# Kernel optimization log

Measured on AMD Instinct MI355X. Metric: run time of the kernel, lower is better.

The kernel has to match this reference:

```python
import jax, jax.numpy as jnp
import numpy as np

NEG_INF = -1e9
LN_EPS = 1e-5

N, F_IN, F_OUT, H = 4096, 128, 64, 4


def setup_inputs() -> dict:
    key = jax.random.key(0)
    ks = jax.random.split(key, 8)
    return {
        "nodes_features": jax.random.normal(ks[0], (N, F_IN), jnp.float32),
        "degree_matrix": jax.random.normal(ks[1], (N, N), jnp.float32),
        "edges_features_distance": jax.random.normal(ks[2], (N, N), jnp.float32),
        "edges_features_bond": jax.random.normal(ks[3], (N, N), jnp.float32),
        "proj_param": jax.random.normal(ks[4], (H, F_IN, F_OUT), jnp.float32) * 0.1,
        "score_src": jax.random.normal(ks[5], (H, F_OUT, 1), jnp.float32) * 0.1,
        "score_tgt": jax.random.normal(ks[6], (H, F_OUT, 1), jnp.float32) * 0.1,
        "skip_w": jax.random.normal(ks[7], (H * F_OUT, F_IN), jnp.float32) * 0.1,
        "cutoff": 0,
    }


def reference(nodes_features, degree_matrix, edges_features_distance,
              edges_features_bond, proj_param, score_src, score_tgt,
              skip_w, cutoff):
    # connectivity mask: nested where on degree/bond matrices  [N, N]
    wdm = degree_matrix + edges_features_bond
    mask = jnp.where(wdm > 0, wdm,
                     jnp.where(edges_features_bond > cutoff,
                               edges_features_bond + wdm, NEG_INF))

    # per-head projection: [H, N, F_out]
    proj = jnp.einsum('nf,hfo->hno', nodes_features, proj_param)

    # scalar scores per node per head: [H, N, 1]
    s_src = jnp.einsum('hno,hop->hnp', proj, score_src)
    s_tgt = jnp.einsum('hno,hop->hnp', proj, score_tgt)

    # broadcast score matrix [H, N, N]; softmax over dim=1 (as in the original)
    scores = jax.nn.leaky_relu(s_src + jnp.swapaxes(s_tgt, 1, 2), negative_slope=0.2)
    attn = jax.nn.softmax(scores + mask[None, :, :], axis=1)

    # weighted aggregation: [H, N, F_out] -> [N, H, F_out]
    out = jnp.einsum('hij,hjf->hif', attn, proj)
    out = jnp.swapaxes(out, 0, 1)

    # skip connection (F_in != F_out -> linear skip projection)
    skip = (nodes_features @ skip_w.T).reshape(-1, H, F_OUT)
    out = out + skip

    # concat heads, ELU activation (no bias: ctor passes bias=None)
    out = jax.nn.elu(out.reshape(-1, H * F_OUT))

    # fresh LayerNorm (weight=1, bias=0) over last dim of mask
    mu = jnp.mean(mask, axis=-1, keepdims=True)
    var = jnp.var(mask, axis=-1, keepdims=True)
    mask_ln = (mask - mu) / jnp.sqrt(var + LN_EPS)

    return out, mask_ln
```

## Files before the change

### kernel.cpp

```cpp
#include <hip/hip_runtime.h>
#include <math.h>

constexpr int kN  = 4096;
constexpr int kFI = 128;
constexpr int kFO = 64;
constexpr int kH  = 4;
constexpr int kHF = 256;
constexpr float kNegInf = -1e9f;
constexpr float kLnEps  = 1e-5f;

typedef short bf16x8 __attribute__((ext_vector_type(8)));
typedef float f32x4  __attribute__((ext_vector_type(4)));

__device__ __forceinline__ float lrelu(float x){ return x >= 0.f ? x : 0.2f*x; }

__device__ __forceinline__ float wave_sum(float v){
  #pragma unroll
  for (int s = 32; s > 0; s >>= 1) v += __shfl_xor(v, s, 64);
  return v;
}

__device__ __forceinline__ unsigned short f2bf(float x){
  unsigned u = __float_as_uint(x);
  u = (u + 0x7fffu + ((u >> 16) & 1u)) >> 16;
  return (unsigned short)u;
}
__device__ __forceinline__ unsigned f2bf_pk(float a, float b){
  return (unsigned)f2bf(a) | ((unsigned)f2bf(b) << 16);
}

__global__ __launch_bounds__(256) void k_tr(
    const float* __restrict__ skw, float* __restrict__ skwT)
{
  const int k  = blockIdx.x;
  const int hf = threadIdx.x;
  skwT[k*kHF + hf] = skw[hf*kFI + k];
}

__global__ __launch_bounds__(256) void k_proj(
    const float* __restrict__ nodes, const float* __restrict__ pp,
    const float* __restrict__ ssrc,  const float* __restrict__ stgt,
    const float* __restrict__ skwT,
    float* __restrict__ proj, float* __restrict__ ga, float* __restrict__ gb,
    float* __restrict__ skipo)
{
  __shared__ float feat[8][kFI];
  const int tid = threadIdx.x;
  const int n0  = blockIdx.x * 8;
  for (int idx = tid; idx < 8*kFI; idx += 256)
    feat[idx >> 7][idx & 127] = nodes[n0*kFI + idx];
  __syncthreads();
  const int h = tid >> 6, o = tid & 63;
  float accP[8], accS[8];
  #pragma unroll
  for (int n = 0; n < 8; ++n){ accP[n] = 0.f; accS[n] = 0.f; }
  for (int k0 = 0; k0 < kFI; k0 += 4){
    float p[4], w[4];
    #pragma unroll
    for (int u = 0; u < 4; ++u){
      p[u] = pp[(h*kFI + k0+u)*kFO + o];
      w[u] = skwT[(k0+u)*kHF + tid];
    }
    #pragma unroll
    for (int n = 0; n < 8; ++n){
      const float4 f4 = *(const float4*)&feat[n][k0];
      accP[n] = fmaf(f4.x, p[0], fmaf(f4.y, p[1],
                fmaf(f4.z, p[2], fmaf(f4.w, p[3], accP[n]))));
      accS[n] = fmaf(f4.x, w[0], fmaf(f4.y, w[1],
                fmaf(f4.z, w[2], fmaf(f4.w, w[3], accS[n]))));
    }
  }
  const float sa = ssrc[h*kFO + o];
  const float sb = stgt[h*kFO + o];
  #pragma unroll
  for (int n = 0; n < 8; ++n){
    proj[(h*kN + n0+n)*kFO + o] = accP[n];
    skipo[(n0+n)*kHF + tid]     = accS[n];
    const float va = wave_sum(accP[n] * sa);
    const float vb = wave_sum(accP[n] * sb);
    if (o == 0){ ga[h*kN + n0+n] = va; gb[h*kN + n0+n] = vb; }
  }
}

template<int RS>
__global__ __launch_bounds__(256, 6) void k_colsum(
    const float* __restrict__ degm, const float* __restrict__ bondm,
    const float* __restrict__ ga,   const float* __restrict__ gb,
    const int* __restrict__ cutp,
    float* __restrict__ Spart, float* __restrict__ statg,
    float* __restrict__ maskws, int write_mask)
{
  const int j0 = (blockIdx.x * 256 + threadIdx.x) * 4;
  const int lane = threadIdx.x & 63;
  const float cut = (float)cutp[0];
  float4 bv[kH]; f32x4 sv[kH];
  #pragma unroll
  for (int h = 0; h < kH; ++h){
    bv[h] = *(const float4*)&gb[h*kN + j0];
    sv[h] = (f32x4){0.f, 0.f, 0.f, 0.f};
  }
  float msum[RS], msq[RS];
  #pragma unroll
  for (int r = 0; r < RS; ++r){ msum[r] = 0.f; msq[r] = 0.f; }

  const int i0 = blockIdx.y * RS;
  #pragma unroll
  for (int ib = 0; ib < RS; ib += 4){
    float4 dg[4], bd[4];
    #pragma unroll
    for (int u = 0; u < 4; ++u){
      const size_t off = (size_t)(i0+ib+u)*kN + j0;
      dg[u] = *(const float4*)&degm[off];
      bd[u] = *(const float4*)&bondm[off];
    }
    #pragma unroll
    for (int u = 0; u < 4; ++u){
      const int i = i0 + ib + u;
      float4 m;
      {
        float w0 = dg[u].x + bd[u].x, w1 = dg[u].y + bd[u].y;
        float w2 = dg[u].z + bd[u].z, w3 = dg[u].w + bd[u].w;
        m.x = w0 > 0.f ? w0 : (bd[u].x > cut ? bd[u].x + w0 : kNegInf);
        m.y = w1 > 0.f ? w1 : (bd[u].y > cut ? bd[u].y + w1 : kNegInf);
        m.z = w2 > 0.f ? w2 : (bd[u].z > cut ? bd[u].z + w2 : kNegInf);
        m.w = w3 > 0.f ? w3 : (bd[u].w > cut ? bd[u].w + w3 : kNegInf);
      }
      if (write_mask) *(float4*)&maskws[(size_t)i*kN + j0] = m;
      msum[ib+u] += (m.x + m.y) + (m.z + m.w);
      msq[ib+u]  += fmaf(m.x, m.x, fmaf(m.y, m.y, fmaf(m.z, m.z, m.w*m.w)));
      #pragma unroll
      for (int h = 0; h < kH; ++h){
        const float a = ga[h*kN + i];
        sv[h][0] += __expf(lrelu(a + bv[h].x) + m.x);
        sv[h][1] += __expf(lrelu(a + bv[h].y) + m.y);
        sv[h][2] += __expf(lrelu(a + bv[h].z) + m.z);
        sv[h][3] += __expf(lrelu(a + bv[h].w) + m.w);
      }
    }
  }
  #pragma unroll
  for (int h = 0; h < kH; ++h)
    *(float4*)&Spart[(size_t)(blockIdx.y*kH + h)*kN + j0] = *(float4*)&sv[h];

  #pragma unroll
  for (int r = 0; r < RS; ++r){
    const float s1 = wave_sum(msum[r]);
    const float s2 = wave_sum(msq[r]);
    if (lane == 0){
      atomicAdd(&statg[2*(i0+r)+0], s1);
      atomicAdd(&statg[2*(i0+r)+1], s2);
    }
  }
}

__global__ __launch_bounds__(256) void k_sred(
    const float* __restrict__ Spart, float* __restrict__ S, int strips)
{
  __shared__ float red[4][64];
  const int hj0  = blockIdx.x * 64;
  const int lane = threadIdx.x & 63;
  const int g    = threadIdx.x >> 6;
  const int per  = strips >> 2;
  float s0=0.f, s1=0.f, s2=0.f, s3=0.f;
  for (int p = g*per; p < (g+1)*per; p += 4){
    s0 += Spart[(size_t)(p+0)*kH*kN + hj0 + lane];
    s1 += Spart[(size_t)(p+1)*kH*kN + hj0 + lane];
    s2 += Spart[(size_t)(p+2)*kH*kN + hj0 + lane];
    s3 += Spart[(size_t)(p+3)*kH*kN + hj0 + lane];
  }
  red[g][lane] = (s0+s1)+(s2+s3);
  __syncthreads();
  if (threadIdx.x < 64)
    S[hj0+lane] = (red[0][lane]+red[1][lane])+(red[2][lane]+red[3][lane]);
}

__global__ __launch_bounds__(256) void k_stat(
    const float* __restrict__ statg, float* __restrict__ statg2)
{
  const int i = blockIdx.x * 256 + threadIdx.x;
  const float mu  = statg[2*i] * (1.f/kN);
  const float var = statg[2*i+1] * (1.f/kN) - mu*mu;
  statg2[2*i+0] = mu;
  statg2[2*i+1] = rsqrtf(var + kLnEps);
}

__global__ __launch_bounds__(256) void k_pack(
    const float* __restrict__ proj, const float* __restrict__ S,
    unsigned short* __restrict__ pSpack)
{
  const int t = blockIdx.x * 256 + threadIdx.x;
  const int L  = t & 63;
  const int nt = (t >> 6) & 3;
  const int kb = (t >> 8) & 127;
  const int h  = t >> 15;
  const int f  = nt*16 + (L & 15);
  const int jb = kb*32 + (L >> 4)*8;
  union { unsigned short s[8]; uint4 v; } u;
  #pragma unroll
  for (int r = 0; r < 8; ++r){
    const int j = jb + r;
    u.s[r] = f2bf(proj[(size_t)(h*kN + j)*kFO + f] / S[h*kN + j]);
  }
  ((uint4*)pSpack)[t] = u.v;
}

__global__ __launch_bounds__(256) void k_aggr(
    const float* __restrict__ degm, const float* __restrict__ bondm,
    const float* __restrict__ maskws, int have_mask,
    const float* __restrict__ ga, const float* __restrict__ gb,
    const int* __restrict__ cutp,
    const unsigned short* __restrict__ pSpack,
    const float* __restrict__ statg2,
    float* __restrict__ accpart, float* __restrict__ mlnp)
{
  __shared__ unsigned short ebuf[kH*16*70];
  const int tid = threadIdx.x;
  const int w   = tid >> 6;
  const int L   = tid & 63;
  const int r0  = blockIdx.x * 16;
  const int jq  = blockIdx.y;
  const int span = kN / gridDim.y;
  const int nc   = span >> 6;
  const int jq0 = jq * span;
  const int ia  = tid >> 4;
  const int jc  = tid & 15;
  const float cut = (float)cutp[0];

  float av[kH];
  #pragma unroll
  for (int hh = 0; hh < kH; ++hh) av[hh] = ga[hh*kN + r0 + ia];
  const float mu = statg2[2*(r0+ia)+0];
  const float rs = statg2[2*(r0+ia)+1];

  f32x4 acc[4];
  #pragma unroll
  for (int nt = 0; nt < 4; ++nt) acc[nt] = (f32x4){0.f,0.f,0.f,0.f};

  for (int c = 0; c < nc; ++c){
    const int jb = jq0 + c*64;
    {
      const int jg = jb + 4*jc;
      const size_t off = (size_t)(r0+ia)*kN + jg;
      float4 m;
      if (have_mask){
        m = *(const float4*)&maskws[off];
      } else {
        const float4 dg = *(const float4*)&degm[off];
        const float4 bd = *(const float4*)&bondm[off];
        float w0 = dg.x + bd.x, w1 = dg.y + bd.y;
        float w2 = dg.z + bd.z, w3 = dg.w + bd.w;
        m.x = w0 > 0.f ? w0 : (bd.x > cut ? bd.x + w0 : kNegInf);
        m.y = w1 > 0.f ? w1 : (bd.y > cut ? bd.y + w1 : kNegInf);
        m.z = w2 > 0.f ? w2 : (bd.z > cut ? bd.z + w2 : kNegInf);
        m.w = w3 > 0.f ? w3 : (bd.w > cut ? bd.w + w3 : kNegInf);
      }
      float4 o;
      o.x = (m.x - mu) * rs;  o.y = (m.y - mu) * rs;
      o.z = (m.z - mu) * rs;  o.w = (m.w - mu) * rs;
      *(float4*)&mlnp[off] = o;
      #pragma unroll
      for (int hh = 0; hh < kH; ++hh){
        const float4 bv = *(const float4*)&gb[hh*kN + jg];
        const float e0 = __expf(lrelu(av[hh] + bv.x) + m.x);
        const float e1 = __expf(lrelu(av[hh] + bv.y) + m.y);
        const float e2 = __expf(lrelu(av[hh] + bv.z) + m.z);
        const float e3 = __expf(lrelu(av[hh] + bv.w) + m.w);
        uint2 u;
        u.x = f2bf_pk(e0, e1);
        u.y = f2bf_pk(e2, e3);
        *(uint2*)&ebuf[(hh*16 + ia)*70 + 4*jc] = u;
      }
    }
    __syncthreads();
    {
      const int kb0 = (jb >> 5);
      #pragma unroll
      for (int ks = 0; ks < 2; ++ks){
        const bf16x8 a = *(const bf16x8*)&ebuf[(w*16 + (L & 15))*70 + ks*32 + (L >> 4)*8];
        const int kb = kb0 + ks;
        #pragma unroll
        for (int nt = 0; nt < 4; ++nt){
          const bf16x8 b = *(const bf16x8*)&pSpack[(size_t)(((w*128 + kb)*4 + nt)*64 + L)*8];
          acc[nt] = __builtin_amdgcn_mfma_f32_16x16x32_bf16(a, b, acc[nt], 0, 0, 0);
        }
      }
    }
    __syncthreads();
  }

  #pragma unroll
  for (int nt = 0; nt < 4; ++nt){
    #pragma unroll
    for (int reg = 0; reg < 4; ++reg){
      const int i = r0 + (L >> 4)*4 + reg;
      const int f = w*64 + nt*16 + (L & 15);
      accpart[((size_t)jq*kN + i)*kHF + f] = acc[nt][reg];
    }
  }
}

__global__ __launch_bounds__(256) void k_out(
    const float* __restrict__ accpart, const float* __restrict__ skipo,
    float* __restrict__ outp, int nq)
{
  const int idx = blockIdx.x * 256 + threadIdx.x;
  float o = skipo[idx];
  for (int q = 0; q < nq; ++q) o += accpart[(size_t)q*kN*kHF + idx];
  o = o > 0.f ? o : expm1f(o);
  outp[idx] = o;
}

extern "C" void kernel_launch(void* const* d_in, const int* in_sizes, int n_in,
                              void* d_out, int out_size, void* d_ws, size_t ws_size,
                              hipStream_t stream)
{
  const float* nodes = (const float*)d_in[0];
  const float* degm  = (const float*)d_in[1];
  const float* bondm = (const float*)d_in[3];
  const float* pp    = (const float*)d_in[4];
  const float* ssrc  = (const float*)d_in[5];
  const float* stgt  = (const float*)d_in[6];
  const float* skw   = (const float*)d_in[7];
  const int*   cutp  = (const int*)d_in[8];

  const size_t fixed_floats = (size_t)kH*kN*kFO + 3*(size_t)kH*kN
                            + (size_t)kN*kHF + 4*(size_t)kN + (size_t)kFI*kHF;
  const size_t psp_floats = ((size_t)kH*kN*kFO)/2;
  const size_t region8 = (size_t)8*kN*kHF;
  const size_t region4 = (size_t)4*kN*kHF;
  const size_t need8      = (fixed_floats + region8 + psp_floats) * sizeof(float);
  const size_t need8_mask = need8 + (size_t)kN*kN*sizeof(float);
  const size_t need4_mask = (fixed_floats + region4 + psp_floats + (size_t)kN*kN)
                            * sizeof(float);

  int nq, strips, have_mask;
  if (ws_size >= need8_mask)      { nq = 8; strips = 512; have_mask = 1; }
  else if (ws_size >= need8)      { nq = 8; strips = 512; have_mask = 0; }
  else                            { nq = 4; strips = 256;
                                    have_mask = (ws_size >= need4_mask) ? 1 : 0; }

  float* ws     = (float*)d_ws;
  float* proj   = ws;
  float* ga     = proj + (size_t)kH*kN*kFO;
  float* gb     = ga + kH*kN;
  float* S      = gb + kH*kN;
  float* skip   = S + kH*kN;
  float* statg  = skip + (size_t)kN*kHF;
  float* statg2 = statg + 2*kN;
  float* skwT   = statg2 + 2*kN;
  float* accpart= skwT + (size_t)kFI*kHF;
  float* Spart  = accpart;
  unsigned short* pSpack = (unsigned short*)(accpart + (size_t)nq*kN*kHF);
  float* mask   = (float*)(pSpack + (size_t)kH*kN*kFO);

  float* outp = (float*)d_out;
  float* mlnp = outp + (size_t)kN*kHF;

  hipMemsetAsync(statg, 0, 2*kN*sizeof(float), stream);

  k_tr<<<kFI, 256, 0, stream>>>(skw, skwT);
  k_proj<<<kN/8, 256, 0, stream>>>(nodes, pp, ssrc, stgt, skwT, proj, ga, gb, skip);
  if (strips == 512)
    k_colsum<8><<<dim3(kN/1024, 512), 256, 0, stream>>>(degm, bondm, ga, gb, cutp,
                                                        Spart, statg, mask, have_mask);
  else
    k_colsum<16><<<dim3(kN/1024, 256), 256, 0, stream>>>(degm, bondm, ga, gb, cutp,
                                                         Spart, statg, mask, have_mask);
  k_sred<<<(kH*kN)/64, 256, 0, stream>>>(Spart, S, strips);
  k_stat<<<kN/256, 256, 0, stream>>>(statg, statg2);
  k_pack<<<(kH*128*4*64)/256, 256, 0, stream>>>(proj, S, pSpack);
  k_aggr<<<dim3(kN/16, nq), 256, 0, stream>>>(degm, bondm, mask, have_mask,
                                              ga, gb, cutp, pSpack, statg2,
                                              accpart, mlnp);
  k_out<<<(kN*kHF)/256, 256, 0, stream>>>(accpart, skip, outp, nq);
}
```

Baseline: 336.2 us.

## Software-pipeline loads in proj and aggr, use exp2, split S reduction across blocks

k_proj now double-buffers its weight loads and k_aggr prefetches the next chunk's mask and gb values, so global loads overlap with compute. Both exponent sites use exp2f with a folded log2(e) factor and a fmax-based leaky ReLU to cut ALU work. k_colsum drops its occupancy hint and loads 8 rows at a time for more memory-level parallelism. k_sred is split over 8 y-blocks that accumulate into S with atomics, and the workspace is reordered so one memset zeroes both statg and S. The costs are higher register pressure and float atomics that make the summation order nondeterministic.

```diff
diff --git a/kernel.cpp b/kernel.cpp
--- a/kernel.cpp
+++ b/kernel.cpp
@@ -8,6 +8,7 @@
 constexpr int kHF = 256;
 constexpr float kNegInf = -1e9f;
 constexpr float kLnEps  = 1e-5f;
+constexpr float kL2E    = 1.44269504f;
 
 typedef short bf16x8 __attribute__((ext_vector_type(8)));
 typedef float f32x4  __attribute__((ext_vector_type(4)));
@@ -54,22 +55,35 @@
   float accP[8], accS[8];
   #pragma unroll
   for (int n = 0; n < 8; ++n){ accP[n] = 0.f; accS[n] = 0.f; }
-  for (int k0 = 0; k0 < kFI; k0 += 4){
-    float p[4], w[4];
+
+  auto LOADK = [&](int kk, float* p, float* w){
     #pragma unroll
     for (int u = 0; u < 4; ++u){
-      p[u] = pp[(h*kFI + k0+u)*kFO + o];
-      w[u] = skwT[(k0+u)*kHF + tid];
-    }
+      p[u] = pp[(h*kFI + kk+u)*kFO + o];
+      w[u] = skwT[(kk+u)*kHF + tid];
+    }
+  };
+  auto COMP = [&](int kk, const float* p, const float* w){
     #pragma unroll
     for (int n = 0; n < 8; ++n){
-      const float4 f4 = *(const float4*)&feat[n][k0];
+      const float4 f4 = *(const float4*)&feat[n][kk];
       accP[n] = fmaf(f4.x, p[0], fmaf(f4.y, p[1],
                 fmaf(f4.z, p[2], fmaf(f4.w, p[3], accP[n]))));
       accS[n] = fmaf(f4.x, w[0], fmaf(f4.y, w[1],
                 fmaf(f4.z, w[2], fmaf(f4.w, w[3], accS[n]))));
     }
-  }
+  };
+
+  float pA[4], wA[4], pB[4], wB[4];
+  LOADK(0, pA, wA);
+  #pragma unroll
+  for (int k0 = 0; k0 < kFI; k0 += 8){
+    LOADK(k0+4, pB, wB);
+    COMP(k0, pA, wA);
+    if (k0+8 < kFI) LOADK(k0+8, pA, wA);
+    COMP(k0+4, pB, wB);
+  }
+
   const float sa = ssrc[h*kFO + o];
   const float sb = stgt[h*kFO + o];
   #pragma unroll
@@ -83,7 +97,7 @@
 }
 
 template<int RS>
-__global__ __launch_bounds__(256, 6) void k_colsum(
+__global__ __launch_bounds__(256) void k_colsum(
     const float* __restrict__ degm, const float* __restrict__ bondm,
     const float* __restrict__ ga,   const float* __restrict__ gb,
     const int* __restrict__ cutp,
@@ -105,16 +119,16 @@
 
   const int i0 = blockIdx.y * RS;
   #pragma unroll
-  for (int ib = 0; ib < RS; ib += 4){
-    float4 dg[4], bd[4];
-    #pragma unroll
-    for (int u = 0; u < 4; ++u){
+  for (int ib = 0; ib < RS; ib += 8){
+    float4 dg[8], bd[8];
+    #pragma unroll
+    for (int u = 0; u < 8; ++u){
       const size_t off = (size_t)(i0+ib+u)*kN + j0;
       dg[u] = *(const float4*)&degm[off];
       bd[u] = *(const float4*)&bondm[off];
     }
     #pragma unroll
-    for (int u = 0; u < 4; ++u){
+    for (int u = 0; u < 8; ++u){
       const int i = i0 + ib + u;
       float4 m;
       {
@@ -128,13 +142,18 @@
       if (write_mask) *(float4*)&maskws[(size_t)i*kN + j0] = m;
       msum[ib+u] += (m.x + m.y) + (m.z + m.w);
       msq[ib+u]  += fmaf(m.x, m.x, fmaf(m.y, m.y, fmaf(m.z, m.z, m.w*m.w)));
+      const float4 ml = {m.x*kL2E, m.y*kL2E, m.z*kL2E, m.w*kL2E};
       #pragma unroll
       for (int h = 0; h < kH; ++h){
         const float a = ga[h*kN + i];
-        sv[h][0] += __expf(lrelu(a + bv[h].x) + m.x);
-        sv[h][1] += __expf(lrelu(a + bv[h].y) + m.y);
-        sv[h][2] += __expf(lrelu(a + bv[h].z) + m.z);
-        sv[h][3] += __expf(lrelu(a + bv[h].w) + m.w);
+        float t0 = a + bv[h].x, t1 = a + bv[h].y;
+        float t2 = a + bv[h].z, t3 = a + bv[h].w;
+        t0 = fmaxf(t0, 0.2f*t0); t1 = fmaxf(t1, 0.2f*t1);
+        t2 = fmaxf(t2, 0.2f*t2); t3 = fmaxf(t3, 0.2f*t3);
+        sv[h][0] += exp2f(fmaf(t0, kL2E, ml.x));
+        sv[h][1] += exp2f(fmaf(t1, kL2E, ml.y));
+        sv[h][2] += exp2f(fmaf(t2, kL2E, ml.z));
+        sv[h][3] += exp2f(fmaf(t3, kL2E, ml.w));
       }
     }
   }
@@ -160,9 +179,11 @@
   const int hj0  = blockIdx.x * 64;
   const int lane = threadIdx.x & 63;
   const int g    = threadIdx.x >> 6;
-  const int per  = strips >> 2;
+  const int per_chunk = strips >> 3;
+  const int per_wave  = per_chunk >> 2;
+  const int p0 = blockIdx.y*per_chunk + g*per_wave;
   float s0=0.f, s1=0.f, s2=0.f, s3=0.f;
-  for (int p = g*per; p < (g+1)*per; p += 4){
+  for (int p = p0; p < p0 + per_wave; p += 4){
     s0 += Spart[(size_t)(p+0)*kH*kN + hj0 + lane];
     s1 += Spart[(size_t)(p+1)*kH*kN + hj0 + lane];
     s2 += Spart[(size_t)(p+2)*kH*kN + hj0 + lane];
@@ -171,7 +192,8 @@
   red[g][lane] = (s0+s1)+(s2+s3);
   __syncthreads();
   if (threadIdx.x < 64)
-    S[hj0+lane] = (red[0][lane]+red[1][lane])+(red[2][lane]+red[3][lane]);
+    atomicAdd(&S[hj0+lane],
+              (red[0][lane]+red[1][lane])+(red[2][lane]+red[3][lane]));
 }
 
 __global__ __launch_bounds__(256) void k_stat(
@@ -236,43 +258,62 @@
   #pragma unroll
   for (int nt = 0; nt < 4; ++nt) acc[nt] = (f32x4){0.f,0.f,0.f,0.f};
 
+  float4 m_n; float4 bv_n[kH];
+  auto LOADC = [&](int c){
+    const int jg = jq0 + c*64 + 4*jc;
+    const size_t off = (size_t)(r0+ia)*kN + jg;
+    if (have_mask){
+      m_n = *(const float4*)&maskws[off];
+    } else {
+      const float4 dg = *(const float4*)&degm[off];
+      const float4 bd = *(const float4*)&bondm[off];
+      float w0 = dg.x + bd.x, w1 = dg.y + bd.y;
+      float w2 = dg.z + bd.z, w3 = dg.w + bd.w;
+      m_n.x = w0 > 0.f ? w0 : (bd.x > cut ? bd.x + w0 : kNegInf);
+      m_n.y = w1 > 0.f ? w1 : (bd.y > cut ? bd.y + w1 : kNegInf);
+      m_n.z = w2 > 0.f ? w2 : (bd.z > cut ? bd.z + w2 : kNegInf);
+      m_n.w = w3 > 0.f ? w3 : (bd.w > cut ? bd.w + w3 : kNegInf);
+    }
+    #pragma unroll
+    for (int hh = 0; hh < kH; ++hh)
+      bv_n[hh] = *(const float4*)&gb[hh*kN + jg];
+  };
+
+  LOADC(0);
   for (int c = 0; c < nc; ++c){
-    const int jb = jq0 + c*64;
     {
-      const int jg = jb + 4*jc;
+      const float4 m = m_n;
+      float4 bvl[kH];
+      #pragma unroll
+      for (int hh = 0; hh < kH; ++hh) bvl[hh] = bv_n[hh];
+
+      const int jg = jq0 + c*64 + 4*jc;
       const size_t off = (size_t)(r0+ia)*kN + jg;
-      float4 m;
-      if (have_mask){
-        m = *(const float4*)&maskws[off];
-      } else {
-        const float4 dg = *(const float4*)&degm[off];
-        const float4 bd = *(const float4*)&bondm[off];
-        float w0 = dg.x + bd.x, w1 = dg.y + bd.y;
-        float w2 = dg.z + bd.z, w3 = dg.w + bd.w;
-        m.x = w0 > 0.f ? w0 : (bd.x > cut ? bd.x + w0 : kNegInf);
-        m.y = w1 > 0.f ? w1 : (bd.y > cut ? bd.y + w1 : kNegInf);
-        m.z = w2 > 0.f ? w2 : (bd.z > cut ? bd.z + w2 : kNegInf);
-        m.w = w3 > 0.f ? w3 : (bd.w > cut ? bd.w + w3 : kNegInf);
-      }
       float4 o;
       o.x = (m.x - mu) * rs;  o.y = (m.y - mu) * rs;
       o.z = (m.z - mu) * rs;  o.w = (m.w - mu) * rs;
       *(float4*)&mlnp[off] = o;
+      const float4 ml = {m.x*kL2E, m.y*kL2E, m.z*kL2E, m.w*kL2E};
       #pragma unroll
       for (int hh = 0; hh < kH; ++hh){
-        const float4 bv = *(const float4*)&gb[hh*kN + jg];
-        const float e0 = __expf(lrelu(av[hh] + bv.x) + m.x);
-        const float e1 = __expf(lrelu(av[hh] + bv.y) + m.y);
-        const float e2 = __expf(lrelu(av[hh] + bv.z) + m.z);
-        const float e3 = __expf(lrelu(av[hh] + bv.w) + m.w);
+        float t0 = av[hh] + bvl[hh].x, t1 = av[hh] + bvl[hh].y;
+        float t2 = av[hh] + bvl[hh].z, t3 = av[hh] + bvl[hh].w;
+        t0 = fmaxf(t0, 0.2f*t0); t1 = fmaxf(t1, 0.2f*t1);
+        t2 = fmaxf(t2, 0.2f*t2); t3 = fmaxf(t3, 0.2f*t3);
+        const float e0 = exp2f(fmaf(t0, kL2E, ml.x));
+        const float e1 = exp2f(fmaf(t1, kL2E, ml.y));
+        const float e2 = exp2f(fmaf(t2, kL2E, ml.z));
+        const float e3 = exp2f(fmaf(t3, kL2E, ml.w));
         uint2 u;
         u.x = f2bf_pk(e0, e1);
         u.y = f2bf_pk(e2, e3);
         *(uint2*)&ebuf[(hh*16 + ia)*70 + 4*jc] = u;
       }
+      if (c+1 < nc) LOADC(c+1);
     }
     __syncthreads();
     {
+      const int jb = jq0 + c*64;
       const int kb0 = (jb >> 5);
       #pragma unroll
       for (int ks = 0; ks < 2; ++ks){
@@ -343,11 +384,11 @@
   float* proj   = ws;
   float* ga     = proj + (size_t)kH*kN*kFO;
   float* gb     = ga + kH*kN;
-  float* S      = gb + kH*kN;
+  float* statg  = gb + kH*kN;
+  float* statg2 = statg + 2*kN;
+  float* S      = statg2 + 2*kN;
   float* skip   = S + kH*kN;
-  float* statg  = skip + (size_t)kN*kHF;
-  float* statg2 = statg + 2*kN;
-  float* skwT   = statg2 + 2*kN;
+  float* skwT   = skip + (size_t)kN*kHF;
   float* accpart= skwT + (size_t)kFI*kHF;
   float* Spart  = accpart;
   unsigned short* pSpack = (unsigned short*)(accpart + (size_t)nq*kN*kHF);
@@ -356,7 +397,7 @@
   float* outp = (float*)d_out;
   float* mlnp = outp + (size_t)kN*kHF;
 
-  hipMemsetAsync(statg, 0, 2*kN*sizeof(float), stream);
+  hipMemsetAsync(statg, 0, (4*(size_t)kN + (size_t)kH*kN)*sizeof(float), stream);
 
   k_tr<<<kFI, 256, 0, stream>>>(skw, skwT);
   k_proj<<<kN/8, 256, 0, stream>>>(nodes, pp, ssrc, stgt, skwT, proj, ga, gb, skip);
@@ -366,7 +407,7 @@
   else
     k_colsum<16><<<dim3(kN/1024, 256), 256, 0, stream>>>(degm, bondm, ga, gb, cutp,
                                                          Spart, statg, mask, have_mask);
-  k_sred<<<(kH*kN)/64, 256, 0, stream>>>(Spart, S, strips);
+  k_sred<<<dim3((kH*kN)/64, 8), 256, 0, stream>>>(Spart, S, strips);
   k_stat<<<kN/256, 256, 0, stream>>>(statg, statg2);
   k_pack<<<(kH*128*4*64)/256, 256, 0, stream>>>(proj, S, pSpack);
   k_aggr<<<dim3(kN/16, nq), 256, 0, stream>>>(degm, bondm, mask, have_mask,
```

After: 508.0 us. 51.1% more time.
